# Optimization experiments

Hardware: AMD Instinct MI355X
Metric: run time of the kernel (lower is better)

The kernel has to match this reference:

```python
import jax, jax.numpy as jnp
import numpy as np

B, P, C = 1024, 64, 512  # batch, patnum, d_model(channels)
LN_EPS = 1e-5

def setup_inputs() -> dict:
    key = jax.random.key(0)
    k = jax.random.split(key, 5)
    s = 1.0 / np.sqrt(P)  # torch Linear default init scale
    x  = jax.random.normal(k[0], (B, P, C), dtype=jnp.float32)
    W1 = jax.random.uniform(k[1], (C, P, P), minval=-s, maxval=s, dtype=jnp.float32)
    b1 = jax.random.uniform(k[2], (C, P),   minval=-s, maxval=s, dtype=jnp.float32)
    W2 = jax.random.uniform(k[3], (C, P, P), minval=-s, maxval=s, dtype=jnp.float32)
    b2 = jax.random.uniform(k[4], (C, P),   minval=-s, maxval=s, dtype=jnp.float32)
    gamma = jnp.ones((C,), dtype=jnp.float32)   # LayerNorm weight
    beta  = jnp.zeros((C,), dtype=jnp.float32)  # LayerNorm bias
    return {"x": x, "W1": W1, "b1": b1, "W2": W2, "b2": b2, "gamma": gamma, "beta": beta}

def reference(x, W1, b1, W2, b2, gamma, beta):
    # Per-channel Linear over the patch dim, batched across channels.
    # torch Linear: y[q] = sum_p x[p] * W[q, p] + b[q]
    h = jnp.einsum('bpc,cqp->bqc', x, W1) + b1.T[None]          # [B, P, C]
    h = jax.nn.gelu(h, approximate=False)                        # exact GELU (torch default)
    o = jnp.einsum('bpc,cqp->bqc', h, W2) + b2.T[None]          # [B, P, C]
    # Dropout is identity in eval; residual + LayerNorm over channel dim.
    res = o + x
    mean = jnp.mean(res, axis=-1, keepdims=True)
    var = jnp.mean((res - mean) ** 2, axis=-1, keepdims=True)
    return (res - mean) * jax.lax.rsqrt(var + LN_EPS) * gamma + beta
```

## Files before the change

kernel.cpp:

```cpp
#include <hip/hip_runtime.h>
#include <cstdint>
#include <cstddef>

#define BB 1024
#define PP 64
#define CC 512
constexpr float LN_EPS = 1e-5f;

typedef short  s16x8 __attribute__((ext_vector_type(8)));
typedef float  f32x4 __attribute__((ext_vector_type(4)));
typedef unsigned int u32x2 __attribute__((ext_vector_type(2)));

__device__ __forceinline__ unsigned cvt_pk_bf16(float lo, float hi) {
    unsigned r;
    asm("v_cvt_pk_bf16_f32 %0, %1, %2" : "=v"(r) : "v"(lo), "v"(hi));
    return r;
}
__device__ __forceinline__ float bflo(unsigned u) { union { unsigned u; float f; } v; v.u = u << 16;          return v.f; }
__device__ __forceinline__ float bfhi(unsigned u) { union { unsigned u; float f; } v; v.u = u & 0xffff0000u;  return v.f; }

__device__ __forceinline__ s16x8 ldwf(const float* p) {
    float4 a = *(const float4*)p;
    float4 b = *(const float4*)(p + 4);
    union { s16x8 v; unsigned u[4]; } r;
    r.u[0] = cvt_pk_bf16(a.x, a.y);
    r.u[1] = cvt_pk_bf16(a.z, a.w);
    r.u[2] = cvt_pk_bf16(b.x, b.y);
    r.u[3] = cvt_pk_bf16(b.z, b.w);
    return r.v;
}

__device__ __forceinline__ float gelu_t(float t) {
    float sg = 1.5957691216f * (t + 0.044715f * t * t * t);
    return t / (1.0f + __expf(-sg));
}

__global__ __launch_bounds__(256, 2) void k_mix(
    const float* __restrict__ X,  const float* __restrict__ W1,
    const float* __restrict__ B1, const float* __restrict__ W2,
    const float* __restrict__ B2, float* __restrict__ OUT)
{
    __shared__ __align__(16) unsigned short XS[4][16][72];
    __shared__ __align__(16) unsigned short HS[4][16][72];
    __shared__ __align__(16) float RS[64][68];

    const int tid  = threadIdx.x;
    const int lane = tid & 63;
    const int wv   = tid >> 6;
    const int lb   = lane & 15;
    const int lq   = lane >> 4;

    const int gid  = blockIdx.x;
    const int xcd  = gid & 7, slot = gid >> 3;
    const int cg   = xcd * 16 + (slot & 15);
    const int bt   = slot >> 4;
    const int c0   = cg * 4, b0 = bt * 128;
    const int c    = c0 + wv;

    const float* w1c = W1 + (size_t)c * 4096;
    const float* w2c = W2 + (size_t)c * 4096;
    const int wq = lb * 64 + lq * 8;
    s16x8 w1_0_0 = ldwf(w1c +    0 + wq), w1_0_1 = ldwf(w1c +    0 + wq + 32);
    s16x8 w1_1_0 = ldwf(w1c + 1024 + wq), w1_1_1 = ldwf(w1c + 1024 + wq + 32);
    s16x8 w1_2_0 = ldwf(w1c + 2048 + wq), w1_2_1 = ldwf(w1c + 2048 + wq + 32);
    s16x8 w1_3_0 = ldwf(w1c + 3072 + wq), w1_3_1 = ldwf(w1c + 3072 + wq + 32);
    s16x8 w2_0_0 = ldwf(w2c +    0 + wq), w2_0_1 = ldwf(w2c +    0 + wq + 32);
    s16x8 w2_1_0 = ldwf(w2c + 1024 + wq), w2_1_1 = ldwf(w2c + 1024 + wq + 32);
    s16x8 w2_2_0 = ldwf(w2c + 2048 + wq), w2_2_1 = ldwf(w2c + 2048 + wq + 32);
    s16x8 w2_3_0 = ldwf(w2c + 3072 + wq), w2_3_1 = ldwf(w2c + 3072 + wq + 32);
    const float4 b1_0 = *(const float4*)(B1 + c * 64 +  0 + lq * 4);
    const float4 b1_1 = *(const float4*)(B1 + c * 64 + 16 + lq * 4);
    const float4 b1_2 = *(const float4*)(B1 + c * 64 + 32 + lq * 4);
    const float4 b1_3 = *(const float4*)(B1 + c * 64 + 48 + lq * 4);
    const float4 b2_0 = *(const float4*)(B2 + c * 64 +  0 + lq * 4);
    const float4 b2_1 = *(const float4*)(B2 + c * 64 + 16 + lq * 4);
    const float4 b2_2 = *(const float4*)(B2 + c * 64 + 32 + lq * 4);
    const float4 b2_3 = *(const float4*)(B2 + c * 64 + 48 + lq * 4);

    const unsigned short* xp = &XS[wv][0][0];
    unsigned short*       hp = &HS[wv][0][0];

    float4 r0[2], r1[2];
    #pragma unroll
    for (int it = 0; it < 2; ++it) {
        int pi = it * 256 + tid;
        int b = pi >> 5, p2 = pi & 31;
        const float* src = X + ((size_t)(b0 + b) * PP + 2 * p2) * CC + c0;
        r0[it] = *(const float4*)src;
        r1[it] = *(const float4*)(src + CC);
    }

    for (int s = 0; s < 8; ++s) {
        const int bb = b0 + s * 16;

        #pragma unroll
        for (int it = 0; it < 2; ++it) {
            int pi = it * 256 + tid;
            int b = pi >> 5, p2 = pi & 31;
            *(unsigned*)&XS[0][b][2 * p2] = cvt_pk_bf16(r0[it].x, r1[it].x);
            *(unsigned*)&XS[1][b][2 * p2] = cvt_pk_bf16(r0[it].y, r1[it].y);
            *(unsigned*)&XS[2][b][2 * p2] = cvt_pk_bf16(r0[it].z, r1[it].z);
            *(unsigned*)&XS[3][b][2 * p2] = cvt_pk_bf16(r0[it].w, r1[it].w);
        }
        __syncthreads();

        if (s < 7) {
            #pragma unroll
            for (int it = 0; it < 2; ++it) {
                int pi = it * 256 + tid;
                int b = pi >> 5, p2 = pi & 31;
                const float* src = X + ((size_t)(bb + 16 + b) * PP + 2 * p2) * CC + c0;
                r0[it] = *(const float4*)src;
                r1[it] = *(const float4*)(src + CC);
            }
        }

        s16x8 xf0 = *(const s16x8*)(xp + lb * 72 +  0 + lq * 8);
        s16x8 xf1 = *(const s16x8*)(xp + lb * 72 + 32 + lq * 8);

        #define DO1(mt) { \
            f32x4 a = {b1_##mt.x, b1_##mt.y, b1_##mt.z, b1_##mt.w}; \
            a = __builtin_amdgcn_mfma_f32_16x16x32_bf16(w1_##mt##_0, xf0, a, 0, 0, 0); \
            a = __builtin_amdgcn_mfma_f32_16x16x32_bf16(w1_##mt##_1, xf1, a, 0, 0, 0); \
            u32x2 h; \
            h[0] = cvt_pk_bf16(gelu_t(a[0]), gelu_t(a[1])); \
            h[1] = cvt_pk_bf16(gelu_t(a[2]), gelu_t(a[3])); \
            *(u32x2*)(hp + lb * 72 + mt * 16 + lq * 4) = h; }
        DO1(0) DO1(1) DO1(2) DO1(3)
        #undef DO1

        asm volatile("s_waitcnt lgkmcnt(0)" ::: "memory");

        s16x8 hf0 = *(const s16x8*)(hp + lb * 72 +  0 + lq * 8);
        s16x8 hf1 = *(const s16x8*)(hp + lb * 72 + 32 + lq * 8);

        #define DO2(mt) { \
            f32x4 a = {b2_##mt.x, b2_##mt.y, b2_##mt.z, b2_##mt.w}; \
            a = __builtin_amdgcn_mfma_f32_16x16x32_bf16(w2_##mt##_0, hf0, a, 0, 0, 0); \
            a = __builtin_amdgcn_mfma_f32_16x16x32_bf16(w2_##mt##_1, hf1, a, 0, 0, 0); \
            u32x2 xv = *(const u32x2*)(xp + lb * 72 + mt * 16 + lq * 4); \
            a[0] += bflo(xv[0]); a[1] += bfhi(xv[0]); \
            a[2] += bflo(xv[1]); a[3] += bfhi(xv[1]); \
            *(f32x4*)&RS[wv * 16 + lb][mt * 16 + lq * 4] = a; }
        DO2(0) DO2(1) DO2(2) DO2(3)
        #undef DO2
        __syncthreads();

        #pragma unroll
        for (int it = 0; it < 4; ++it) {
            int fi = it * 256 + tid;
            int q = fi & 63, b = fi >> 6;
            float4 v = { RS[b][q], RS[16 + b][q], RS[32 + b][q], RS[48 + b][q] };
            *(float4*)(OUT + ((size_t)(bb + b) * PP + q) * CC + c0) = v;
        }
    }
}

__global__ __launch_bounds__(256) void k_ln(
    float* __restrict__ OUT, const float* __restrict__ G, const float* __restrict__ Be)
{
    const int lane = threadIdx.x & 63;
    const int m    = blockIdx.x * 4 + (threadIdx.x >> 6);
    float4* row = (float4*)(OUT + (size_t)m * CC);
    float4 v0 = row[lane], v1 = row[lane + 64];
    float s = (v0.x + v0.y) + (v0.z + v0.w) + (v1.x + v1.y) + (v1.z + v1.w);
    float q = (v0.x * v0.x + v0.y * v0.y) + (v0.z * v0.z + v0.w * v0.w)
            + (v1.x * v1.x + v1.y * v1.y) + (v1.z * v1.z + v1.w * v1.w);
    #pragma unroll
    for (int o = 32; o >= 1; o >>= 1) {
        s += __shfl_xor(s, o, 64);
        q += __shfl_xor(q, o, 64);
    }
    const float mu  = s * (1.0f / CC);
    const float var = q * (1.0f / CC) - mu * mu;
    const float inv = rsqrtf(var + LN_EPS);
    const float4 g0 = ((const float4*)G)[lane],  g1 = ((const float4*)G)[lane + 64];
    const float4 e0 = ((const float4*)Be)[lane], e1 = ((const float4*)Be)[lane + 64];
    v0.x = (v0.x - mu) * inv * g0.x + e0.x;  v0.y = (v0.y - mu) * inv * g0.y + e0.y;
    v0.z = (v0.z - mu) * inv * g0.z + e0.z;  v0.w = (v0.w - mu) * inv * g0.w + e0.w;
    v1.x = (v1.x - mu) * inv * g1.x + e1.x;  v1.y = (v1.y - mu) * inv * g1.y + e1.y;
    v1.z = (v1.z - mu) * inv * g1.z + e1.z;  v1.w = (v1.w - mu) * inv * g1.w + e1.w;
    row[lane] = v0; row[lane + 64] = v1;
}

extern "C" void kernel_launch(void* const* d_in, const int* in_sizes, int n_in,
                              void* d_out, int out_size, void* d_ws, size_t ws_size,
                              hipStream_t stream) {
    const float* X  = (const float*)d_in[0];
    const float* W1 = (const float*)d_in[1];
    const float* B1 = (const float*)d_in[2];
    const float* W2 = (const float*)d_in[3];
    const float* B2 = (const float*)d_in[4];
    const float* G  = (const float*)d_in[5];
    const float* Be = (const float*)d_in[6];
    float* OUT = (float*)d_out;

    k_mix<<<1024, 256, 0, stream>>>(X, W1, B1, W2, B2, OUT);
    k_ln<<<(BB * PP) / 4, 256, 0, stream>>>(OUT, G, Be);
}
```

Measured before the change: 348.0 us.

## Widen mixing block to 16 channels for coalesced X loads and output stores

Each k_mix block now covers 16 channels with 1024 threads (16 waves) instead of 4 channels with 256 threads, and the grid shrinks to 256 blocks. Each X row read and OUT row write now spans 64 contiguous bytes instead of 16, which should cut wasted memory transactions on the strided fp32 access. Per-channel biases move from registers into shared memory. The LDS tiles are re-laid-out to match, and the XCD-aware block swizzle is dropped. The cost is a larger LDS footprint and a tighter per-thread register budget at 1024 threads, which could cause spills, plus only one block per CU.

```diff
diff --git a/kernel.cpp b/kernel.cpp
--- a/kernel.cpp
+++ b/kernel.cpp
@@ -35,14 +35,15 @@
     return t / (1.0f + __expf(-sg));
 }
 
-__global__ __launch_bounds__(256, 2) void k_mix(
+__global__ __launch_bounds__(1024) void k_mix(
     const float* __restrict__ X,  const float* __restrict__ W1,
     const float* __restrict__ B1, const float* __restrict__ W2,
     const float* __restrict__ B2, float* __restrict__ OUT)
 {
-    __shared__ __align__(16) unsigned short XS[4][16][72];
-    __shared__ __align__(16) unsigned short HS[4][16][72];
-    __shared__ __align__(16) float RS[64][68];
+    __shared__ __align__(16) unsigned short XS[16 * 1160];
+    __shared__ __align__(16) unsigned short HS[16 * 1152];
+    __shared__ __align__(16) float          RS[16 * 1092];
+    __shared__ __align__(16) float          BS[16 * 128];
 
     const int tid  = threadIdx.x;
     const int lane = tid & 63;
@@ -50,12 +51,11 @@
     const int lb   = lane & 15;
     const int lq   = lane >> 4;
 
-    const int gid  = blockIdx.x;
-    const int xcd  = gid & 7, slot = gid >> 3;
-    const int cg   = xcd * 16 + (slot & 15);
-    const int bt   = slot >> 4;
-    const int c0   = cg * 4, b0 = bt * 128;
-    const int c    = c0 + wv;
+    const int gid = blockIdx.x;
+    const int cg  = gid & 31;
+    const int bt  = gid >> 5;
+    const int c0  = cg * 16, b0 = bt * 128;
+    const int c   = c0 + wv;
 
     const float* w1c = W1 + (size_t)c * 4096;
     const float* w2c = W2 + (size_t)c * 4096;
@@ -68,50 +68,46 @@
     s16x8 w2_1_0 = ldwf(w2c + 1024 + wq), w2_1_1 = ldwf(w2c + 1024 + wq + 32);
     s16x8 w2_2_0 = ldwf(w2c + 2048 + wq), w2_2_1 = ldwf(w2c + 2048 + wq + 32);
     s16x8 w2_3_0 = ldwf(w2c + 3072 + wq), w2_3_1 = ldwf(w2c + 3072 + wq + 32);
-    const float4 b1_0 = *(const float4*)(B1 + c * 64 +  0 + lq * 4);
-    const float4 b1_1 = *(const float4*)(B1 + c * 64 + 16 + lq * 4);
-    const float4 b1_2 = *(const float4*)(B1 + c * 64 + 32 + lq * 4);
-    const float4 b1_3 = *(const float4*)(B1 + c * 64 + 48 + lq * 4);
-    const float4 b2_0 = *(const float4*)(B2 + c * 64 +  0 + lq * 4);
-    const float4 b2_1 = *(const float4*)(B2 + c * 64 + 16 + lq * 4);
-    const float4 b2_2 = *(const float4*)(B2 + c * 64 + 32 + lq * 4);
-    const float4 b2_3 = *(const float4*)(B2 + c * 64 + 48 + lq * 4);
 
-    const unsigned short* xp = &XS[wv][0][0];
-    unsigned short*       hp = &HS[wv][0][0];
+    BS[wv * 128 +      lane] = B1[c * 64 + lane];
+    BS[wv * 128 + 64 + lane] = B2[c * 64 + lane];
+
+    const unsigned short* xp = &XS[wv * 1160];
+    unsigned short*       hp = &HS[wv * 1152];
+
+    const int sc4 = tid & 3;
+    const int sp2 = (tid >> 2) & 31;
+    const int sbo = tid >> 7;
 
     float4 r0[2], r1[2];
     #pragma unroll
-    for (int it = 0; it < 2; ++it) {
-        int pi = it * 256 + tid;
-        int b = pi >> 5, p2 = pi & 31;
-        const float* src = X + ((size_t)(b0 + b) * PP + 2 * p2) * CC + c0;
-        r0[it] = *(const float4*)src;
-        r1[it] = *(const float4*)(src + CC);
+    for (int pass = 0; pass < 2; ++pass) {
+        const float* src = X + ((size_t)(b0 + pass * 8 + sbo) * PP + 2 * sp2) * CC
+                             + c0 + sc4 * 4;
+        r0[pass] = *(const float4*)src;
+        r1[pass] = *(const float4*)(src + CC);
     }
 
     for (int s = 0; s < 8; ++s) {
         const int bb = b0 + s * 16;
 
         #pragma unroll
-        for (int it = 0; it < 2; ++it) {
-            int pi = it * 256 + tid;
-            int b = pi >> 5, p2 = pi & 31;
-            *(unsigned*)&XS[0][b][2 * p2] = cvt_pk_bf16(r0[it].x, r1[it].x);
-            *(unsigned*)&XS[1][b][2 * p2] = cvt_pk_bf16(r0[it].y, r1[it].y);
-            *(unsigned*)&XS[2][b][2 * p2] = cvt_pk_bf16(r0[it].z, r1[it].z);
-            *(unsigned*)&XS[3][b][2 * p2] = cvt_pk_bf16(r0[it].w, r1[it].w);
+        for (int pass = 0; pass < 2; ++pass) {
+            int b = pass * 8 + sbo;
+            *(unsigned*)&XS[(sc4 * 4 + 0) * 1160 + b * 72 + 2 * sp2] = cvt_pk_bf16(r0[pass].x, r1[pass].x);
+            *(unsigned*)&XS[(sc4 * 4 + 1) * 1160 + b * 72 + 2 * sp2] = cvt_pk_bf16(r0[pass].y, r1[pass].y);
+            *(unsigned*)&XS[(sc4 * 4 + 2) * 1160 + b * 72 + 2 * sp2] = cvt_pk_bf16(r0[pass].z, r1[pass].z);
+            *(unsigned*)&XS[(sc4 * 4 + 3) * 1160 + b * 72 + 2 * sp2] = cvt_pk_bf16(r0[pass].w, r1[pass].w);
         }
         __syncthreads();
 
         if (s < 7) {
             #pragma unroll
-            for (int it = 0; it < 2; ++it) {
-                int pi = it * 256 + tid;
-                int b = pi >> 5, p2 = pi & 31;
-                const float* src = X + ((size_t)(bb + 16 + b) * PP + 2 * p2) * CC + c0;
-                r0[it] = *(const float4*)src;
-                r1[it] = *(const float4*)(src + CC);
+            for (int pass = 0; pass < 2; ++pass) {
+                const float* src = X + ((size_t)(bb + 16 + pass * 8 + sbo) * PP + 2 * sp2) * CC
+                                     + c0 + sc4 * 4;
+                r0[pass] = *(const float4*)src;
+                r1[pass] = *(const float4*)(src + CC);
             }
         }
 
@@ -119,7 +115,8 @@
         s16x8 xf1 = *(const s16x8*)(xp + lb * 72 + 32 + lq * 8);
 
         #define DO1(mt) { \
-            f32x4 a = {b1_##mt.x, b1_##mt.y, b1_##mt.z, b1_##mt.w}; \
+            float4 bv = *(const float4*)&BS[wv * 128 + mt * 16 + lq * 4]; \
+            f32x4 a = {bv.x, bv.y, bv.z, bv.w}; \
             a = __builtin_amdgcn_mfma_f32_16x16x32_bf16(w1_##mt##_0, xf0, a, 0, 0, 0); \
             a = __builtin_amdgcn_mfma_f32_16x16x32_bf16(w1_##mt##_1, xf1, a, 0, 0, 0); \
             u32x2 h; \
@@ -135,23 +132,25 @@
         s16x8 hf1 = *(const s16x8*)(hp + lb * 72 + 32 + lq * 8);
 
         #define DO2(mt) { \
-            f32x4 a = {b2_##mt.x, b2_##mt.y, b2_##mt.z, b2_##mt.w}; \
+            float4 bv = *(const float4*)&BS[wv * 128 + 64 + mt * 16 + lq * 4]; \
+            f32x4 a = {bv.x, bv.y, bv.z, bv.w}; \
             a = __builtin_amdgcn_mfma_f32_16x16x32_bf16(w2_##mt##_0, hf0, a, 0, 0, 0); \
             a = __builtin_amdgcn_mfma_f32_16x16x32_bf16(w2_##mt##_1, hf1, a, 0, 0, 0); \
             u32x2 xv = *(const u32x2*)(xp + lb * 72 + mt * 16 + lq * 4); \
             a[0] += bflo(xv[0]); a[1] += bfhi(xv[0]); \
             a[2] += bflo(xv[1]); a[3] += bfhi(xv[1]); \
-            *(f32x4*)&RS[wv * 16 + lb][mt * 16 + lq * 4] = a; }
+            *(f32x4*)&RS[lb * 1092 + wv * 68 + mt * 16 + lq * 4] = a; }
         DO2(0) DO2(1) DO2(2) DO2(3)
         #undef DO2
         __syncthreads();
 
         #pragma unroll
         for (int it = 0; it < 4; ++it) {
-            int fi = it * 256 + tid;
-            int q = fi & 63, b = fi >> 6;
-            float4 v = { RS[b][q], RS[16 + b][q], RS[32 + b][q], RS[48 + b][q] };
-            *(float4*)(OUT + ((size_t)(bb + b) * PP + q) * CC + c0) = v;
+            int fi = it * 1024 + tid;
+            int c4 = fi & 3, q = (fi >> 2) & 63, b = fi >> 8;
+            const float* rp = &RS[b * 1092 + c4 * 4 * 68 + q];
+            float4 v = { rp[0], rp[68], rp[136], rp[204] };
+            *(float4*)(OUT + ((size_t)(bb + b) * PP + q) * CC + c0 + c4 * 4) = v;
         }
     }
 }
@@ -195,6 +194,6 @@
     const float* Be = (const float*)d_in[6];
     float* OUT = (float*)d_out;
 
-    k_mix<<<1024, 256, 0, stream>>>(X, W1, B1, W2, B2, OUT);
+    k_mix<<<256, 1024, 0, stream>>>(X, W1, B1, W2, B2, OUT);
     k_ln<<<(BB * PP) / 4, 256, 0, stream>>>(OUT, G, Be);
 }
```

After: 340.3 us. 2.2% less time.
